# Performance work log

Hardware: AMD Instinct MI355X
Metric: run time of the kernel (lower is better)

## Reference

```python
import jax, jax.numpy as jnp
import numpy as np

B, L, E = 16, 1022, 1280
D, H, FF, NL = 512, 8, 2048, 4
DH = D // H
EPS = 1e-5


def layer_norm(x, s, b):
    m = jnp.mean(x, axis=-1, keepdims=True)
    v = jnp.mean(jnp.square(x - m), axis=-1, keepdims=True)
    return (x - m) * jax.lax.rsqrt(v + EPS) * s + b


def setup_inputs() -> dict:
    key = jax.random.key(0)
    ks = jax.random.split(key, 12)
    s = 0.02
    return {
        "embeddings": jax.random.normal(ks[0], (B, L, E), jnp.float32),
        "mask": jnp.ones((B, L), jnp.float32),
        "position": jnp.tile(jnp.arange(L, dtype=jnp.int32)[None, :], (B, 1)),
        "proj_w": jax.random.normal(ks[1], (D, E), jnp.float32) * s,
        "proj_b": jnp.zeros((D,), jnp.float32),
        "proj_ln_s": jnp.ones((D,), jnp.float32),
        "proj_ln_b": jnp.zeros((D,), jnp.float32),
        "ln1_s": jnp.ones((NL, D), jnp.float32),
        "ln1_b": jnp.zeros((NL, D), jnp.float32),
        "in_w": jax.random.normal(ks[2], (NL, 3 * D, D), jnp.float32) * s,
        "in_b": jnp.zeros((NL, 3 * D), jnp.float32),
        "out_w": jax.random.normal(ks[3], (NL, D, D), jnp.float32) * s,
        "out_b": jnp.zeros((NL, D), jnp.float32),
        "ln2_s": jnp.ones((NL, D), jnp.float32),
        "ln2_b": jnp.zeros((NL, D), jnp.float32),
        "w1": jax.random.normal(ks[4], (NL, FF, D), jnp.float32) * s,
        "b1": jnp.zeros((NL, FF), jnp.float32),
        "w2": jax.random.normal(ks[5], (NL, D, FF), jnp.float32) * s,
        "b2": jnp.zeros((NL, D), jnp.float32),
        "h1_w": jax.random.normal(ks[6], (128, 2 * D), jnp.float32) * s,
        "h1_b": jnp.zeros((128,), jnp.float32),
        "hln_s": jnp.ones((128,), jnp.float32),
        "hln_b": jnp.zeros((128,), jnp.float32),
        "h2_w": jax.random.normal(ks[7], (1, 128), jnp.float32) * s,
        "h2_b": jnp.zeros((1,), jnp.float32),
    }


def _rope_tables():
    inv_freq = 1.0 / (10000.0 ** (jnp.arange(0, DH, 2, dtype=jnp.float32) / DH))
    t = jnp.arange(L, dtype=jnp.float32)
    freqs = jnp.outer(t, inv_freq)          # [L, DH/2]
    emb = jnp.concatenate([freqs, freqs], axis=-1)  # [L, DH]
    return jnp.cos(emb), jnp.sin(emb)


def _rotate_half(x):
    x1, x2 = jnp.split(x, 2, axis=-1)
    return jnp.concatenate([-x2, x1], axis=-1)


def _apply_rope(x, cos, sin):
    # x: [B, L, D] -> per-head rotation -> [B, L, D]
    xh = x.reshape(B, L, H, DH)
    xh = xh * cos[None, :, None, :] + _rotate_half(xh) * sin[None, :, None, :]
    return xh.reshape(B, L, D)


def _forward(embeddings, mask, proj_w, proj_b, proj_ln_s, proj_ln_b,
             ln1_s, ln1_b, in_w, in_b, out_w, out_b, ln2_s, ln2_b,
             w1, b1, w2, b2, h1_w, h1_b, hln_s, hln_b, h2_w, h2_b):
    cos, sin = _rope_tables()
    x = layer_norm(embeddings @ proj_w.T + proj_b, proj_ln_s, proj_ln_b)  # [B,L,D]
    pad = mask <= 0  # True where padded (~mask.bool())
    scale = 1.0 / jnp.sqrt(jnp.float32(DH))
    for i in range(NL):
        n = layer_norm(x, ln1_s[i], ln1_b[i])
        q_in = _apply_rope(n, cos, sin)
        k_in = _apply_rope(n, cos, sin)
        v_in = n
        wq, wk, wv = jnp.split(in_w[i], 3, axis=0)
        bq, bk, bv = jnp.split(in_b[i], 3, axis=0)
        qh = (q_in @ wq.T + bq).reshape(B, L, H, DH)
        kh = (k_in @ wk.T + bk).reshape(B, L, H, DH)
        vh = (v_in @ wv.T + bv).reshape(B, L, H, DH)
        scores = jnp.einsum('blhd,bmhd->bhlm', qh, kh) * scale
        scores = jnp.where(pad[:, None, None, :], jnp.float32(-1e9), scores)
        attn = jax.nn.softmax(scores, axis=-1)
        o = jnp.einsum('bhlm,bmhd->blhd', attn, vh).reshape(B, L, D)
        x = x + (o @ out_w[i].T + out_b[i])
        n2 = layer_norm(x, ln2_s[i], ln2_b[i])
        x = x + (jax.nn.relu(n2 @ w1[i].T + b1[i]) @ w2[i].T + b2[i])
    # masked mean pool
    gctx = (x * mask[..., None]).sum(axis=1) / mask.sum(axis=1, keepdims=True)  # [B,D]
    combined = jnp.concatenate([x, jnp.broadcast_to(gctx[:, None, :], (B, L, D))], axis=-1)
    h = jax.nn.relu(layer_norm(combined @ h1_w.T + h1_b, hln_s, hln_b))
    logits = (h @ h2_w.T + h2_b).squeeze(-1)  # [B,L]
    return logits


def reference(embeddings, mask, position, proj_w, proj_b, proj_ln_s, proj_ln_b,
              ln1_s, ln1_b, in_w, in_b, out_w, out_b, ln2_s, ln2_b,
              w1, b1, w2, b2, h1_w, h1_b, hln_s, hln_b, h2_w, h2_b):
    # position is accepted for API parity but unused (as in the torch module)
    return _forward(embeddings, mask, proj_w, proj_b, proj_ln_s, proj_ln_b,
                    ln1_s, ln1_b, in_w, in_b, out_w, out_b, ln2_s, ln2_b,
                    w1, b1, w2, b2, h1_w, h1_b, hln_s, hln_b, h2_w, h2_b)
```

## Files before the change

kernel.cpp:

```cpp
#include <hip/hip_runtime.h>
#include <cstdint>
#include <cstddef>

#define B_   16
#define L_   1022
#define E_   1280
#define D_   512
#define H_   8
#define FF_  2048
#define NL_  4
#define DH_  64
#define BL_  (B_*L_)
#define EPS_ 1e-5f

typedef unsigned short u16;
typedef unsigned int   u32;
typedef float f32x4 __attribute__((ext_vector_type(4)));
typedef short s16x8 __attribute__((ext_vector_type(8)));

__device__ __forceinline__ u16 f2bf(float f) {
    u32 u = __builtin_bit_cast(u32, f);
    u += 0x7fffu + ((u >> 16) & 1u);
    return (u16)(u >> 16);
}
__device__ __forceinline__ float bf2f(u16 u) {
    return __builtin_bit_cast(float, (u32)u << 16);
}

__global__ __launch_bounds__(256)
void cast_k(const float* __restrict__ src, u16* __restrict__ dst, int n8) {
    int t = blockIdx.x * 256 + threadIdx.x;
    if (t >= n8) return;
    const float* s = src + (size_t)t * 8;
    float4 a = *(const float4*)(s);
    float4 b = *(const float4*)(s + 4);
    s16x8 o;
    o[0] = (short)f2bf(a.x); o[1] = (short)f2bf(a.y);
    o[2] = (short)f2bf(a.z); o[3] = (short)f2bf(a.w);
    o[4] = (short)f2bf(b.x); o[5] = (short)f2bf(b.y);
    o[6] = (short)f2bf(b.z); o[7] = (short)f2bf(b.w);
    *(s16x8*)(dst + (size_t)t * 8) = o;
}

__global__ __launch_bounds__(256)
void h1cast_k(const float* __restrict__ src, u16* __restrict__ dst) {
    int t = blockIdx.x * 256 + threadIdx.x;
    if (t >= 128 * 512 / 8) return;
    int row = t >> 6, c8 = (t & 63) << 3;
    const float* s = src + (size_t)row * 1024 + c8;
    float4 a = *(const float4*)(s);
    float4 b = *(const float4*)(s + 4);
    s16x8 o;
    o[0] = (short)f2bf(a.x); o[1] = (short)f2bf(a.y);
    o[2] = (short)f2bf(a.z); o[3] = (short)f2bf(a.w);
    o[4] = (short)f2bf(b.x); o[5] = (short)f2bf(b.y);
    o[6] = (short)f2bf(b.z); o[7] = (short)f2bf(b.w);
    *(s16x8*)(dst + (size_t)row * 512 + c8) = o;
}

__global__ void tables_k(float* __restrict__ ct, float* __restrict__ st) {
    int idx = blockIdx.x * blockDim.x + threadIdx.x;
    if (idx >= L_ * DH_) return;
    int l = idx / DH_;
    int d = idx % DH_;
    int j = d & 31;
    float invf = powf(10000.0f, -(float)(2 * j) / (float)DH_);
    float ang = (float)l * invf;
    ct[idx] = cosf(ang);
    st[idx] = sinf(ang);
}

template<bool RELU, bool RESID, bool OUTBF, bool ROWBIAS>
__global__ __launch_bounds__(256)
void mgemm_k(const u16* __restrict__ A, const u16* __restrict__ W,
             const float* __restrict__ bias, const float* __restrict__ resid,
             void* __restrict__ Cout, int M, int N, int K)
{
    constexpr int LDT = 72;
    __shared__ u16 As[128 * LDT];
    __shared__ u16 Ws[128 * LDT];
    const int nt = N >> 7;
    const int bx = blockIdx.x % nt;
    const int by = blockIdx.x / nt;
    const int m0 = by << 7, n0 = bx << 7;
    const int tid = threadIdx.x;
    const int lane = tid & 63, wid = tid >> 6;
    const int wr = wid >> 1, wc = wid & 1;
    const int lr = lane & 15, lk = lane >> 4;

    f32x4 acc[4][4];
#pragma unroll
    for (int m = 0; m < 4; m++)
#pragma unroll
        for (int n = 0; n < 4; n++) acc[m][n] = (f32x4)0.0f;

    for (int k0 = 0; k0 < K; k0 += 64) {
        s16x8 va[4], vw[4];
#pragma unroll
        for (int u = 0; u < 4; u++) {
            int ch = tid + (u << 8);
            int r = ch >> 3, c8 = (ch & 7) << 3;
            int ar = m0 + r; if (ar >= M) ar = M - 1;
            va[u] = *(const s16x8*)(A + (size_t)ar * K + k0 + c8);
            vw[u] = *(const s16x8*)(W + (size_t)(n0 + r) * K + k0 + c8);
        }
        __syncthreads();
#pragma unroll
        for (int u = 0; u < 4; u++) {
            int ch = tid + (u << 8);
            int r = ch >> 3, c8 = (ch & 7) << 3;
            *(s16x8*)&As[r * LDT + c8] = va[u];
            *(s16x8*)&Ws[r * LDT + c8] = vw[u];
        }
        __syncthreads();
#pragma unroll
        for (int kk = 0; kk < 2; kk++) {
            s16x8 af[4], bf[4];
#pragma unroll
            for (int m = 0; m < 4; m++)
                af[m] = *(const s16x8*)&As[(wr * 64 + m * 16 + lr) * LDT + kk * 32 + lk * 8];
#pragma unroll
            for (int n = 0; n < 4; n++)
                bf[n] = *(const s16x8*)&Ws[(wc * 64 + n * 16 + lr) * LDT + kk * 32 + lk * 8];
#pragma unroll
            for (int m = 0; m < 4; m++)
#pragma unroll
                for (int n = 0; n < 4; n++)
                    acc[m][n] = __builtin_amdgcn_mfma_f32_16x16x32_bf16(
                        af[m], bf[n], acc[m][n], 0, 0, 0);
        }
    }

    float bv[4];
    if constexpr (!ROWBIAS) {
#pragma unroll
        for (int n = 0; n < 4; n++) bv[n] = bias[n0 + wc * 64 + n * 16 + lr];
    }
#pragma unroll
    for (int m = 0; m < 4; m++) {
#pragma unroll
        for (int j = 0; j < 4; j++) {
            int row = m0 + wr * 64 + m * 16 + lk * 4 + j;
            if (row >= M) continue;
            const float* rb = nullptr;
            if constexpr (ROWBIAS) rb = bias + (size_t)(row / L_) * N;
#pragma unroll
            for (int n = 0; n < 4; n++) {
                int col = n0 + wc * 64 + n * 16 + lr;
                float c = acc[m][n][j];
                if constexpr (ROWBIAS) c += rb[col];
                else                   c += bv[n];
                if constexpr (RELU) c = fmaxf(c, 0.0f);
                if constexpr (RESID) c += resid[(size_t)row * N + col];
                if constexpr (OUTBF) ((u16*)Cout)[(size_t)row * N + col] = f2bf(c);
                else                 ((float*)Cout)[(size_t)row * N + col] = c;
            }
        }
    }
}

template<int DD, bool RELU, bool OUTBF>
__global__ __launch_bounds__(256)
void ln_k(const float* __restrict__ x, const float* __restrict__ s,
          const float* __restrict__ bb, void* __restrict__ out, int M)
{
    const int lane = threadIdx.x & 63;
    const int row = (blockIdx.x << 2) + (threadIdx.x >> 6);
    if (row >= M) return;
    const float* xr = x + (size_t)row * DD;
    constexpr int NV = DD / 64;
    float v[NV];
    if constexpr (NV == 8) {
        *(float4*)(v)     = *(const float4*)(xr + lane * 8);
        *(float4*)(v + 4) = *(const float4*)(xr + lane * 8 + 4);
    } else {
        float2 t = *(const float2*)(xr + lane * 2);
        v[0] = t.x; v[1] = t.y;
    }
    float sum = 0.f, sq = 0.f;
#pragma unroll
    for (int e = 0; e < NV; e++) { sum += v[e]; sq += v[e] * v[e]; }
#pragma unroll
    for (int msk = 1; msk < 64; msk <<= 1) {
        sum += __shfl_xor(sum, msk);
        sq  += __shfl_xor(sq, msk);
    }
    const float mean = sum * (1.0f / DD);
    const float var  = sq * (1.0f / DD) - mean * mean;
    const float rstd = rsqrtf(var + EPS_);
#pragma unroll
    for (int e = 0; e < NV; e++) {
        int d = lane * NV + e;
        float r = (v[e] - mean) * rstd * s[d] + bb[d];
        if constexpr (RELU) r = fmaxf(r, 0.0f);
        v[e] = r;
    }
    if constexpr (OUTBF) {
        u16* orow = (u16*)out + (size_t)row * DD;
        if constexpr (NV == 8) {
            s16x8 o;
#pragma unroll
            for (int e = 0; e < 8; e++) o[e] = (short)f2bf(v[e]);
            *(s16x8*)(orow + lane * 8) = o;
        } else {
            orow[lane * 2] = f2bf(v[0]); orow[lane * 2 + 1] = f2bf(v[1]);
        }
    } else {
        float* orow = (float*)out + (size_t)row * DD;
        if constexpr (NV == 8) {
            *(float4*)(orow + lane * 8)     = *(float4*)(v);
            *(float4*)(orow + lane * 8 + 4) = *(float4*)(v + 4);
        } else {
            float2 t; t.x = v[0]; t.y = v[1];
            *(float2*)(orow + lane * 2) = t;
        }
    }
}

__global__ __launch_bounds__(256)
void rope_k(const u16* __restrict__ n, const float* __restrict__ ct,
            const float* __restrict__ st, u16* __restrict__ r)
{
    int t = blockIdx.x * 256 + threadIdx.x;
    if (t >= BL_ * D_ / 8) return;
    int idx = t << 3;
    int l = (idx / D_) % L_;
    int d = idx & (D_ - 1);
    int dd = d & 63;
    s16x8 xv = *(const s16x8*)(n + idx);
    int pidx; float sgn;
    if (dd < 32) { pidx = idx + 32; sgn = -1.0f; }
    else         { pidx = idx - 32; sgn =  1.0f; }
    s16x8 pv = *(const s16x8*)(n + pidx);
    float4 c0 = *(const float4*)(ct + l * DH_ + dd);
    float4 c1 = *(const float4*)(ct + l * DH_ + dd + 4);
    float4 s0 = *(const float4*)(st + l * DH_ + dd);
    float4 s1 = *(const float4*)(st + l * DH_ + dd + 4);
    float cc[8] = {c0.x,c0.y,c0.z,c0.w,c1.x,c1.y,c1.z,c1.w};
    float ss[8] = {s0.x,s0.y,s0.z,s0.w,s1.x,s1.y,s1.z,s1.w};
    s16x8 o;
#pragma unroll
    for (int e = 0; e < 8; e++) {
        float xf = bf2f((u16)xv[e]);
        float pf = bf2f((u16)pv[e]);
        o[e] = (short)f2bf(xf * cc[e] + sgn * pf * ss[e]);
    }
    *(s16x8*)(r + idx) = o;
}

__global__ __launch_bounds__(256)
void attn_k(const u16* __restrict__ q, const u16* __restrict__ kk_,
            const u16* __restrict__ v, const float* __restrict__ mask,
            u16* __restrict__ o)
{
    constexpr int LDA = 68;
    __shared__ u16 Kt[64 * LDA];
    __shared__ u16 Vt[64 * LDA];
    __shared__ u16 Pl[64 * LDA];
    const int bh = blockIdx.x >> 4, qt = blockIdx.x & 15;
    const int b = bh >> 3, h = bh & 7;
    const int tid = threadIdx.x;
    const int lane = tid & 63, w = tid >> 6;
    const int lr = lane & 15, lg = lane >> 4;
    const size_t basebl = (size_t)b * L_;

    const int qrow = qt * 64 + w * 16 + lr;
    const int qclamp = qrow < L_ ? qrow : L_ - 1;
    s16x8 aq[2];
#pragma unroll
    for (int kk = 0; kk < 2; kk++)
        aq[kk] = *(const s16x8*)(q + (basebl + qclamp) * D_ + h * DH_ + kk * 32 + lg * 8);

    f32x4 oacc[4];
    float m_run[4], l_run[4];
#pragma unroll
    for (int n = 0; n < 4; n++) oacc[n] = (f32x4)0.0f;
#pragma unroll
    for (int j = 0; j < 4; j++) { m_run[j] = -1e30f; l_run[j] = 0.f; }

    for (int kt = 0; kt < 16; kt++) {
        __syncthreads();
#pragma unroll
        for (int u = 0; u < 2; u++) {
            int ch = tid + (u << 8);
            int key = ch >> 3, d8 = (ch & 7) << 3;
            int gk = kt * 64 + key;
            int gkc = gk < L_ ? gk : L_ - 1;
            s16x8 kv = *(const s16x8*)(kk_ + (basebl + gkc) * D_ + h * DH_ + d8);
            s16x8 vv = *(const s16x8*)(v   + (basebl + gkc) * D_ + h * DH_ + d8);
            *(s16x8*)&Kt[key * LDA + d8] = kv;
#pragma unroll
            for (int e = 0; e < 8; e++) Vt[(d8 + e) * LDA + key] = (u16)vv[e];
        }
        __syncthreads();

        f32x4 sacc[4];
#pragma unroll
        for (int n = 0; n < 4; n++) {
            sacc[n] = (f32x4)0.0f;
#pragma unroll
            for (int kk = 0; kk < 2; kk++) {
                s16x8 bk = *(const s16x8*)&Kt[(n * 16 + lr) * LDA + kk * 32 + lg * 8];
                sacc[n] = __builtin_amdgcn_mfma_f32_16x16x32_bf16(aq[kk], bk, sacc[n], 0, 0, 0);
            }
        }
        bool val[4];
#pragma unroll
        for (int n = 0; n < 4; n++) {
            int key = kt * 64 + n * 16 + lr;
            val[n] = (key < L_) && (mask[basebl + key] > 0.0f);
        }
#pragma unroll
        for (int j = 0; j < 4; j++) {
            float sv[4];
#pragma unroll
            for (int n = 0; n < 4; n++)
                sv[n] = val[n] ? sacc[n][j] * 0.125f : -1e30f;
            float tm = fmaxf(fmaxf(sv[0], sv[1]), fmaxf(sv[2], sv[3]));
#pragma unroll
            for (int msk = 1; msk <= 8; msk <<= 1) tm = fmaxf(tm, __shfl_xor(tm, msk));
            float nm = fmaxf(m_run[j], tm);
            float corr = __expf(m_run[j] - nm);
            m_run[j] = nm;
            float p[4], ts = 0.f;
#pragma unroll
            for (int n = 0; n < 4; n++) { p[n] = __expf(sv[n] - nm); ts += p[n]; }
#pragma unroll
            for (int msk = 1; msk <= 8; msk <<= 1) ts += __shfl_xor(ts, msk);
            l_run[j] = l_run[j] * corr + ts;
#pragma unroll
            for (int n = 0; n < 4; n++) {
                oacc[n][j] *= corr;
                Pl[(w * 16 + lg * 4 + j) * LDA + n * 16 + lr] = f2bf(p[n]);
            }
        }
#pragma unroll
        for (int kk = 0; kk < 2; kk++) {
            s16x8 ap = *(const s16x8*)&Pl[(w * 16 + lr) * LDA + kk * 32 + lg * 8];
#pragma unroll
            for (int n = 0; n < 4; n++) {
                s16x8 bv = *(const s16x8*)&Vt[(n * 16 + lr) * LDA + kk * 32 + lg * 8];
                oacc[n] = __builtin_amdgcn_mfma_f32_16x16x32_bf16(ap, bv, oacc[n], 0, 0, 0);
            }
        }
    }

#pragma unroll
    for (int j = 0; j < 4; j++) {
        int qr = qt * 64 + w * 16 + lg * 4 + j;
        if (qr >= L_) continue;
        float inv = 1.0f / l_run[j];
#pragma unroll
        for (int n = 0; n < 4; n++)
            o[(basebl + qr) * D_ + h * DH_ + n * 16 + lr] = f2bf(oacc[n][j] * inv);
    }
}

__global__ __launch_bounds__(512)
void pool_k(const float* __restrict__ x, const float* __restrict__ mask,
             float* __restrict__ g)
{
    const int b = blockIdx.x;
    const int d = threadIdx.x;
    float acc = 0.f, ms = 0.f;
    for (int l = 0; l < L_; l++) {
        float mv = mask[b * L_ + l];
        acc += x[((size_t)b * L_ + l) * D_ + d] * mv;
        ms += mv;
    }
    g[b * D_ + d] = acc / ms;
}

__global__ __launch_bounds__(256)
void gpart_k(const float* __restrict__ g, const float* __restrict__ h1w,
             const float* __restrict__ h1b, float* __restrict__ gp)
{
    const int lane = threadIdx.x & 63;
    const int gid = (blockIdx.x << 2) + (threadIdx.x >> 6);
    const int b = gid >> 7, j = gid & 127;
    const float* wr = h1w + (size_t)j * (2 * D_) + D_;
    const float* gr = g + b * D_;
    float4 a0 = *(const float4*)(gr + lane * 8);
    float4 a1 = *(const float4*)(gr + lane * 8 + 4);
    float4 w0 = *(const float4*)(wr + lane * 8);
    float4 w1v = *(const float4*)(wr + lane * 8 + 4);
    float acc = a0.x * w0.x + a0.y * w0.y + a0.z * w0.z + a0.w * w0.w
              + a1.x * w1v.x + a1.y * w1v.y + a1.z * w1v.z + a1.w * w1v.w;
#pragma unroll
    for (int msk = 1; msk < 64; msk <<= 1) acc += __shfl_xor(acc, msk);
    if (lane == 0) gp[b * 128 + j] = acc + h1b[j];
}

__global__ __launch_bounds__(256)
void logits_k(const float* __restrict__ h, const float* __restrict__ w,
              const float* __restrict__ bsc, float* __restrict__ out, int M)
{
    const int lane = threadIdx.x & 63;
    const int row = (blockIdx.x << 2) + (threadIdx.x >> 6);
    if (row >= M) return;
    float2 hv = *(const float2*)(h + (size_t)row * 128 + lane * 2);
    float2 wv = *(const float2*)(w + lane * 2);
    float acc = hv.x * wv.x + hv.y * wv.y;
#pragma unroll
    for (int msk = 1; msk < 64; msk <<= 1) acc += __shfl_xor(acc, msk);
    if (lane == 0) out[row] = acc + bsc[0];
}

extern "C" void kernel_launch(void* const* d_in, const int* in_sizes, int n_in,
                              void* d_out, int out_size, void* d_ws, size_t ws_size,
                              hipStream_t stream)
{
    const float* emb       = (const float*)d_in[0];
    const float* mask      = (const float*)d_in[1];
    const float* proj_w    = (const float*)d_in[3];
    const float* proj_b    = (const float*)d_in[4];
    const float* proj_ln_s = (const float*)d_in[5];
    const float* proj_ln_b = (const float*)d_in[6];
    const float* ln1_s     = (const float*)d_in[7];
    const float* ln1_b     = (const float*)d_in[8];
    const float* in_w      = (const float*)d_in[9];
    const float* in_b      = (const float*)d_in[10];
    const float* out_w     = (const float*)d_in[11];
    const float* out_b     = (const float*)d_in[12];
    const float* ln2_s     = (const float*)d_in[13];
    const float* ln2_b     = (const float*)d_in[14];
    const float* w1        = (const float*)d_in[15];
    const float* b1        = (const float*)d_in[16];
    const float* w2        = (const float*)d_in[17];
    const float* b2        = (const float*)d_in[18];
    const float* h1_w      = (const float*)d_in[19];
    const float* h1_b      = (const float*)d_in[20];
    const float* hln_s     = (const float*)d_in[21];
    const float* hln_b     = (const float*)d_in[22];
    const float* h2_w      = (const float*)d_in[23];
    const float* h2_b      = (const float*)d_in[24];
    float* out = (float*)d_out;

    float* ws = (float*)d_ws;
    const size_t S = (size_t)BL_ * D_;
    float* X  = ws;
    float* Rf = ws + S;
    u16* QB    = (u16*)(ws + S);
    u16* KB    = (u16*)(ws + S) + S;
    u16* VB    = (u16*)(ws + 2 * S);
    u16* NbB   = (u16*)(ws + 2 * S) + S;
    u16* FFb16 = (u16*)(ws + 3 * S);
    u16* RopeB = FFb16;
    u16* embB  = FFb16;
    u16* RB    = (u16*)(ws + 4 * S);
    u16* projwB = (u16*)(ws + 5 * S);
    u16* iwB  = projwB + 512 * 1280;
    u16* owB  = iwB + (size_t)NL_ * 3 * D_ * D_;
    u16* w1B  = owB + (size_t)NL_ * D_ * D_;
    u16* w2B  = w1B + (size_t)NL_ * FF_ * D_;
    u16* h1wB = w2B + (size_t)NL_ * D_ * FF_;
    float* CT = ws + 5 * S + 6651904;
    float* ST = CT + L_ * DH_;
    float* GC = ST + L_ * DH_;
    float* GP = GC + B_ * D_;
    float* Hb = Rf;

    const int MT = 128;
    const dim3 blk(256);
    const int lnGrid = (BL_ + 3) / 4;

    cast_k<<<(BL_ * E_ / 8 + 255) / 256, blk, 0, stream>>>(emb, embB, BL_ * E_ / 8);
    cast_k<<<(512 * 1280 / 8 + 255) / 256, blk, 0, stream>>>(proj_w, projwB, 512 * 1280 / 8);
    cast_k<<<(NL_ * 3 * D_ * D_ / 8 + 255) / 256, blk, 0, stream>>>(in_w, iwB, NL_ * 3 * D_ * D_ / 8);
    cast_k<<<(NL_ * D_ * D_ / 8 + 255) / 256, blk, 0, stream>>>(out_w, owB, NL_ * D_ * D_ / 8);
    cast_k<<<(NL_ * FF_ * D_ / 8 + 255) / 256, blk, 0, stream>>>(w1, w1B, NL_ * FF_ * D_ / 8);
    cast_k<<<(NL_ * D_ * FF_ / 8 + 255) / 256, blk, 0, stream>>>(w2, w2B, NL_ * D_ * FF_ / 8);
    h1cast_k<<<(128 * 512 / 8 + 255) / 256, blk, 0, stream>>>(h1_w, h1wB);
    tables_k<<<(L_ * DH_ + 255) / 256, blk, 0, stream>>>(CT, ST);

    mgemm_k<false,false,false,false><<<MT * (D_ / 128), blk, 0, stream>>>(
        embB, projwB, proj_b, nullptr, Rf, BL_, D_, E_);
    ln_k<D_,false,false><<<lnGrid, blk, 0, stream>>>(Rf, proj_ln_s, proj_ln_b, X, BL_);

    for (int i = 0; i < NL_; i++) {
        const u16* iw = iwB + (size_t)i * 3 * D_ * D_;
        const float* ib = in_b + (size_t)i * 3 * D_;
        ln_k<D_,false,true><<<lnGrid, blk, 0, stream>>>(X, ln1_s + i * D_, ln1_b + i * D_, NbB, BL_);
        mgemm_k<false,false,true,false><<<MT * 4, blk, 0, stream>>>(
            NbB, iw + 2 * D_ * D_, ib + 2 * D_, nullptr, VB, BL_, D_, D_);
        rope_k<<<(BL_ * D_ / 8 + 255) / 256, blk, 0, stream>>>(NbB, CT, ST, RopeB);
        mgemm_k<false,false,true,false><<<MT * 4, blk, 0, stream>>>(
            RopeB, iw, ib, nullptr, QB, BL_, D_, D_);
        mgemm_k<false,false,true,false><<<MT * 4, blk, 0, stream>>>(
            RopeB, iw + D_ * D_, ib + D_, nullptr, KB, BL_, D_, D_);
        attn_k<<<B_ * H_ * 16, blk, 0, stream>>>(QB, KB, VB, mask, RB);
        mgemm_k<false,true,false,false><<<MT * 4, blk, 0, stream>>>(
            RB, owB + (size_t)i * D_ * D_, out_b + i * D_, X, X, BL_, D_, D_);
        ln_k<D_,false,true><<<lnGrid, blk, 0, stream>>>(X, ln2_s + i * D_, ln2_b + i * D_, NbB, BL_);
        mgemm_k<true,false,true,false><<<MT * 16, blk, 0, stream>>>(
            NbB, w1B + (size_t)i * FF_ * D_, b1 + i * FF_, nullptr, FFb16, BL_, FF_, D_);
        mgemm_k<false,true,false,false><<<MT * 4, blk, 0, stream>>>(
            FFb16, w2B + (size_t)i * D_ * FF_, b2 + i * D_, X, X, BL_, D_, FF_);
    }

    pool_k<<<B_, dim3(512), 0, stream>>>(X, mask, GC);
    gpart_k<<<(B_ * 128) / 4, blk, 0, stream>>>(GC, h1_w, h1_b, GP);
    cast_k<<<(int)((S / 8 + 255) / 256), blk, 0, stream>>>(X, NbB, (int)(S / 8));
    mgemm_k<false,false,false,true><<<MT * 1, blk, 0, stream>>>(
        NbB, h1wB, GP, nullptr, Hb, BL_, 128, D_);
    ln_k<128,true,false><<<lnGrid, blk, 0, stream>>>(Hb, hln_s, hln_b, Hb, BL_);
    logits_k<<<lnGrid, blk, 0, stream>>>(Hb, h2_w, h2_b, out, BL_);
}
```

Before: 1.579 ms.

## Use direct global-to-LDS loads in GEMM, fuse Q/K projections, prefetch attention tiles

The GEMM now stages A and W tiles with global_load_lds straight into unpadded shared memory, skipping the register round trip. The separate Q and K projection GEMMs become one N=1024 GEMM writing an interleaved QK buffer, which saves a launch and re-reading the activations. The attention kernel prefetches the next K/V tile into registers while computing on the current one. The unpadded 64-wide LDS rows may cause bank conflicts on fragment reads, and the loads now sit right after the barrier instead of before it.

```diff
diff --git a/kernel.cpp b/kernel.cpp
--- a/kernel.cpp
+++ b/kernel.cpp
@@ -25,6 +25,13 @@
 }
 __device__ __forceinline__ float bf2f(u16 u) {
     return __builtin_bit_cast(float, (u32)u << 16);
+}
+
+__device__ __forceinline__ void gload_lds16(const u16* g, u16* l) {
+    __builtin_amdgcn_global_load_lds(
+        (const __attribute__((address_space(1))) void*)g,
+        (__attribute__((address_space(3))) void*)l,
+        16, 0, 0);
 }
 
 __global__ __launch_bounds__(256)
@@ -76,9 +83,8 @@
              const float* __restrict__ bias, const float* __restrict__ resid,
              void* __restrict__ Cout, int M, int N, int K)
 {
-    constexpr int LDT = 72;
-    __shared__ u16 As[128 * LDT];
-    __shared__ u16 Ws[128 * LDT];
+    __shared__ u16 As[128 * 64];
+    __shared__ u16 Ws[128 * 64];
     const int nt = N >> 7;
     const int bx = blockIdx.x % nt;
     const int by = blockIdx.x / nt;
@@ -95,22 +101,14 @@
         for (int n = 0; n < 4; n++) acc[m][n] = (f32x4)0.0f;
 
     for (int k0 = 0; k0 < K; k0 += 64) {
-        s16x8 va[4], vw[4];
+        __syncthreads();
 #pragma unroll
         for (int u = 0; u < 4; u++) {
             int ch = tid + (u << 8);
             int r = ch >> 3, c8 = (ch & 7) << 3;
             int ar = m0 + r; if (ar >= M) ar = M - 1;
-            va[u] = *(const s16x8*)(A + (size_t)ar * K + k0 + c8);
-            vw[u] = *(const s16x8*)(W + (size_t)(n0 + r) * K + k0 + c8);
-        }
-        __syncthreads();
-#pragma unroll
-        for (int u = 0; u < 4; u++) {
-            int ch = tid + (u << 8);
-            int r = ch >> 3, c8 = (ch & 7) << 3;
-            *(s16x8*)&As[r * LDT + c8] = va[u];
-            *(s16x8*)&Ws[r * LDT + c8] = vw[u];
+            gload_lds16(A + (size_t)ar * K + k0 + c8, &As[ch * 8]);
+            gload_lds16(W + (size_t)(n0 + r) * K + k0 + c8, &Ws[ch * 8]);
         }
         __syncthreads();
 #pragma unroll
@@ -118,10 +116,10 @@
             s16x8 af[4], bf[4];
 #pragma unroll
             for (int m = 0; m < 4; m++)
-                af[m] = *(const s16x8*)&As[(wr * 64 + m * 16 + lr) * LDT + kk * 32 + lk * 8];
+                af[m] = *(const s16x8*)&As[(wr * 64 + m * 16 + lr) * 64 + kk * 32 + lk * 8];
 #pragma unroll
             for (int n = 0; n < 4; n++)
-                bf[n] = *(const s16x8*)&Ws[(wc * 64 + n * 16 + lr) * LDT + kk * 32 + lk * 8];
+                bf[n] = *(const s16x8*)&Ws[(wc * 64 + n * 16 + lr) * 64 + kk * 32 + lk * 8];
 #pragma unroll
             for (int m = 0; m < 4; m++)
 #pragma unroll
@@ -249,9 +247,8 @@
 }
 
 __global__ __launch_bounds__(256)
-void attn_k(const u16* __restrict__ q, const u16* __restrict__ kk_,
-            const u16* __restrict__ v, const float* __restrict__ mask,
-            u16* __restrict__ o)
+void attn_k(const u16* __restrict__ qk, const u16* __restrict__ v,
+            const float* __restrict__ mask, u16* __restrict__ o)
 {
     constexpr int LDA = 68;
     __shared__ u16 Kt[64 * LDA];
@@ -269,7 +266,17 @@
     s16x8 aq[2];
 #pragma unroll
     for (int kk = 0; kk < 2; kk++)
-        aq[kk] = *(const s16x8*)(q + (basebl + qclamp) * D_ + h * DH_ + kk * 32 + lg * 8);
+        aq[kk] = *(const s16x8*)(qk + (basebl + qclamp) * 1024 + h * DH_ + kk * 32 + lg * 8);
+
+    s16x8 kreg[2], vreg[2];
+    const int pch_key[2] = { tid >> 3, (tid + 256) >> 3 };
+    const int pch_d8 = (tid & 7) << 3;
+#pragma unroll
+    for (int u = 0; u < 2; u++) {
+        int gk = pch_key[u]; if (gk >= L_) gk = L_ - 1;
+        kreg[u] = *(const s16x8*)(qk + (basebl + gk) * 1024 + 512 + h * DH_ + pch_d8);
+        vreg[u] = *(const s16x8*)(v  + (basebl + gk) * D_ + h * DH_ + pch_d8);
+    }
 
     f32x4 oacc[4];
     float m_run[4], l_run[4];
@@ -282,17 +289,19 @@
         __syncthreads();
 #pragma unroll
         for (int u = 0; u < 2; u++) {
-            int ch = tid + (u << 8);
-            int key = ch >> 3, d8 = (ch & 7) << 3;
-            int gk = kt * 64 + key;
-            int gkc = gk < L_ ? gk : L_ - 1;
-            s16x8 kv = *(const s16x8*)(kk_ + (basebl + gkc) * D_ + h * DH_ + d8);
-            s16x8 vv = *(const s16x8*)(v   + (basebl + gkc) * D_ + h * DH_ + d8);
-            *(s16x8*)&Kt[key * LDA + d8] = kv;
-#pragma unroll
-            for (int e = 0; e < 8; e++) Vt[(d8 + e) * LDA + key] = (u16)vv[e];
+            *(s16x8*)&Kt[pch_key[u] * LDA + pch_d8] = kreg[u];
+#pragma unroll
+            for (int e = 0; e < 8; e++) Vt[(pch_d8 + e) * LDA + pch_key[u]] = (u16)vreg[u][e];
         }
         __syncthreads();
+        if (kt < 15) {
+#pragma unroll
+            for (int u = 0; u < 2; u++) {
+                int gk = (kt + 1) * 64 + pch_key[u]; if (gk >= L_) gk = L_ - 1;
+                kreg[u] = *(const s16x8*)(qk + (basebl + gk) * 1024 + 512 + h * DH_ + pch_d8);
+                vreg[u] = *(const s16x8*)(v  + (basebl + gk) * D_ + h * DH_ + pch_d8);
+            }
+        }
 
         f32x4 sacc[4];
 #pragma unroll
@@ -440,8 +449,7 @@
     const size_t S = (size_t)BL_ * D_;
     float* X  = ws;
     float* Rf = ws + S;
-    u16* QB    = (u16*)(ws + S);
-    u16* KB    = (u16*)(ws + S) + S;
+    u16* QKB   = (u16*)(ws + S);
     u16* VB    = (u16*)(ws + 2 * S);
     u16* NbB   = (u16*)(ws + 2 * S) + S;
     u16* FFb16 = (u16*)(ws + 3 * S);
@@ -484,11 +492,9 @@
         mgemm_k<false,false,true,false><<<MT * 4, blk, 0, stream>>>(
             NbB, iw + 2 * D_ * D_, ib + 2 * D_, nullptr, VB, BL_, D_, D_);
         rope_k<<<(BL_ * D_ / 8 + 255) / 256, blk, 0, stream>>>(NbB, CT, ST, RopeB);
-        mgemm_k<false,false,true,false><<<MT * 4, blk, 0, stream>>>(
-            RopeB, iw, ib, nullptr, QB, BL_, D_, D_);
-        mgemm_k<false,false,true,false><<<MT * 4, blk, 0, stream>>>(
-            RopeB, iw + D_ * D_, ib + D_, nullptr, KB, BL_, D_, D_);
-        attn_k<<<B_ * H_ * 16, blk, 0, stream>>>(QB, KB, VB, mask, RB);
+        mgemm_k<false,false,true,false><<<MT * 8, blk, 0, stream>>>(
+            RopeB, iw, ib, nullptr, QKB, BL_, 1024, D_);
+        attn_k<<<B_ * H_ * 16, blk, 0, stream>>>(QKB, VB, mask, RB);
         mgemm_k<false,true,false,false><<<MT * 4, blk, 0, stream>>>(
             RB, owB + (size_t)i * D_ * D_, out_b + i * D_, X, X, BL_, D_, D_);
         ln_k<D_,false,true><<<lnGrid, blk, 0, stream>>>(X, ln2_s + i * D_, ln2_b + i * D_, NbB, BL_);
```

New measurement: 1.705 ms. +8.0%, slower.

## Fuse Q/K projections into one GEMM and process two query tiles per attention block

Applied to the files above, without the earlier changes.

The separate Q and K projection GEMMs become a single N=1024 GEMM writing an interleaved QK buffer. The attention kernel now handles 128 query rows per block (two 16-row groups per wave), so each staged K/V tile is reused twice and the kernel launches half as many blocks. The softmax row sum is no longer computed with shuffle reductions; an extra MFMA against a vector of ones accumulates it instead. The trade-offs are more registers per thread, fewer blocks to fill the GPU, and a denominator taken from bf16-rounded probabilities.

```diff
diff --git a/kernel.cpp b/kernel.cpp
--- a/kernel.cpp
+++ b/kernel.cpp
@@ -249,110 +249,124 @@
 }
 
 __global__ __launch_bounds__(256)
-void attn_k(const u16* __restrict__ q, const u16* __restrict__ kk_,
-            const u16* __restrict__ v, const float* __restrict__ mask,
-            u16* __restrict__ o)
+void attn_k(const u16* __restrict__ qk, const u16* __restrict__ v,
+            const float* __restrict__ mask, u16* __restrict__ o)
 {
     constexpr int LDA = 68;
     __shared__ u16 Kt[64 * LDA];
     __shared__ u16 Vt[64 * LDA];
     __shared__ u16 Pl[64 * LDA];
-    const int bh = blockIdx.x >> 4, qt = blockIdx.x & 15;
+    const int bh = blockIdx.x >> 3, qt = blockIdx.x & 7;
     const int b = bh >> 3, h = bh & 7;
     const int tid = threadIdx.x;
     const int lane = tid & 63, w = tid >> 6;
     const int lr = lane & 15, lg = lane >> 4;
     const size_t basebl = (size_t)b * L_;
 
-    const int qrow = qt * 64 + w * 16 + lr;
-    const int qclamp = qrow < L_ ? qrow : L_ - 1;
-    s16x8 aq[2];
-#pragma unroll
-    for (int kk = 0; kk < 2; kk++)
-        aq[kk] = *(const s16x8*)(q + (basebl + qclamp) * D_ + h * DH_ + kk * 32 + lg * 8);
-
-    f32x4 oacc[4];
-    float m_run[4], l_run[4];
-#pragma unroll
-    for (int n = 0; n < 4; n++) oacc[n] = (f32x4)0.0f;
-#pragma unroll
-    for (int j = 0; j < 4; j++) { m_run[j] = -1e30f; l_run[j] = 0.f; }
+    s16x8 aq[2][2];
+#pragma unroll
+    for (int g = 0; g < 2; g++) {
+        int qrow = qt * 128 + w * 32 + g * 16 + lr;
+        int qc = qrow < L_ ? qrow : L_ - 1;
+#pragma unroll
+        for (int kk = 0; kk < 2; kk++)
+            aq[g][kk] = *(const s16x8*)(qk + (basebl + qc) * 1024 + h * DH_ + kk * 32 + lg * 8);
+    }
+
+    s16x8 bones;
+#pragma unroll
+    for (int e = 0; e < 8; e++) bones[e] = (short)0x3F80;
+
+    f32x4 oacc[2][4], ocs[2];
+    float m_run[2][4];
+#pragma unroll
+    for (int g = 0; g < 2; g++) {
+        ocs[g] = (f32x4)0.0f;
+#pragma unroll
+        for (int n = 0; n < 4; n++) oacc[g][n] = (f32x4)0.0f;
+#pragma unroll
+        for (int j = 0; j < 4; j++) m_run[g][j] = -1e30f;
+    }
+
+    const int st_key = tid >> 3;
+    const int st_d8 = (tid & 7) << 3;
 
     for (int kt = 0; kt < 16; kt++) {
         __syncthreads();
 #pragma unroll
         for (int u = 0; u < 2; u++) {
-            int ch = tid + (u << 8);
-            int key = ch >> 3, d8 = (ch & 7) << 3;
-            int gk = kt * 64 + key;
-            int gkc = gk < L_ ? gk : L_ - 1;
-            s16x8 kv = *(const s16x8*)(kk_ + (basebl + gkc) * D_ + h * DH_ + d8);
-            s16x8 vv = *(const s16x8*)(v   + (basebl + gkc) * D_ + h * DH_ + d8);
-            *(s16x8*)&Kt[key * LDA + d8] = kv;
-#pragma unroll
-            for (int e = 0; e < 8; e++) Vt[(d8 + e) * LDA + key] = (u16)vv[e];
+            int key = st_key + u * 32;
+            int gk = kt * 64 + key; if (gk >= L_) gk = L_ - 1;
+            s16x8 kv = *(const s16x8*)(qk + (basebl + gk) * 1024 + 512 + h * DH_ + st_d8);
+            s16x8 vv = *(const s16x8*)(v  + (basebl + gk) * D_ + h * DH_ + st_d8);
+            *(s16x8*)&Kt[key * LDA + st_d8] = kv;
+#pragma unroll
+            for (int e = 0; e < 8; e++) Vt[(st_d8 + e) * LDA + key] = (u16)vv[e];
         }
         __syncthreads();
 
-        f32x4 sacc[4];
-#pragma unroll
-        for (int n = 0; n < 4; n++) {
-            sacc[n] = (f32x4)0.0f;
-#pragma unroll
-            for (int kk = 0; kk < 2; kk++) {
-                s16x8 bk = *(const s16x8*)&Kt[(n * 16 + lr) * LDA + kk * 32 + lg * 8];
-                sacc[n] = __builtin_amdgcn_mfma_f32_16x16x32_bf16(aq[kk], bk, sacc[n], 0, 0, 0);
-            }
-        }
         bool val[4];
 #pragma unroll
         for (int n = 0; n < 4; n++) {
             int key = kt * 64 + n * 16 + lr;
             val[n] = (key < L_) && (mask[basebl + key] > 0.0f);
         }
+
+#pragma unroll
+        for (int g = 0; g < 2; g++) {
+            f32x4 sacc[4];
+#pragma unroll
+            for (int n = 0; n < 4; n++) {
+                sacc[n] = (f32x4)0.0f;
+#pragma unroll
+                for (int kk = 0; kk < 2; kk++) {
+                    s16x8 bk = *(const s16x8*)&Kt[(n * 16 + lr) * LDA + kk * 32 + lg * 8];
+                    sacc[n] = __builtin_amdgcn_mfma_f32_16x16x32_bf16(aq[g][kk], bk, sacc[n], 0, 0, 0);
+                }
+            }
+#pragma unroll
+            for (int j = 0; j < 4; j++) {
+                float sv[4];
+#pragma unroll
+                for (int n = 0; n < 4; n++)
+                    sv[n] = val[n] ? sacc[n][j] * 0.125f : -1e30f;
+                float tm = fmaxf(fmaxf(sv[0], sv[1]), fmaxf(sv[2], sv[3]));
+#pragma unroll
+                for (int msk = 1; msk <= 8; msk <<= 1) tm = fmaxf(tm, __shfl_xor(tm, msk));
+                float nm = fmaxf(m_run[g][j], tm);
+                float corr = __expf(m_run[g][j] - nm);
+                m_run[g][j] = nm;
+                ocs[g][j] *= corr;
+#pragma unroll
+                for (int n = 0; n < 4; n++) {
+                    oacc[g][n][j] *= corr;
+                    Pl[(w * 16 + lg * 4 + j) * LDA + n * 16 + lr] = f2bf(__expf(sv[n] - nm));
+                }
+            }
+#pragma unroll
+            for (int kk = 0; kk < 2; kk++) {
+                s16x8 ap = *(const s16x8*)&Pl[(w * 16 + lr) * LDA + kk * 32 + lg * 8];
+#pragma unroll
+                for (int n = 0; n < 4; n++) {
+                    s16x8 bv = *(const s16x8*)&Vt[(n * 16 + lr) * LDA + kk * 32 + lg * 8];
+                    oacc[g][n] = __builtin_amdgcn_mfma_f32_16x16x32_bf16(ap, bv, oacc[g][n], 0, 0, 0);
+                }
+                ocs[g] = __builtin_amdgcn_mfma_f32_16x16x32_bf16(ap, bones, ocs[g], 0, 0, 0);
+            }
+        }
+    }
+
+#pragma unroll
+    for (int g = 0; g < 2; g++) {
 #pragma unroll
         for (int j = 0; j < 4; j++) {
-            float sv[4];
+            int qr = qt * 128 + w * 32 + g * 16 + lg * 4 + j;
+            if (qr >= L_) continue;
+            float inv = 1.0f / ocs[g][j];
 #pragma unroll
             for (int n = 0; n < 4; n++)
-                sv[n] = val[n] ? sacc[n][j] * 0.125f : -1e30f;
-            float tm = fmaxf(fmaxf(sv[0], sv[1]), fmaxf(sv[2], sv[3]));
-#pragma unroll
-            for (int msk = 1; msk <= 8; msk <<= 1) tm = fmaxf(tm, __shfl_xor(tm, msk));
-            float nm = fmaxf(m_run[j], tm);
-            float corr = __expf(m_run[j] - nm);
-            m_run[j] = nm;
-            float p[4], ts = 0.f;
-#pragma unroll
-            for (int n = 0; n < 4; n++) { p[n] = __expf(sv[n] - nm); ts += p[n]; }
-#pragma unroll
-            for (int msk = 1; msk <= 8; msk <<= 1) ts += __shfl_xor(ts, msk);
-            l_run[j] = l_run[j] * corr + ts;
-#pragma unroll
-            for (int n = 0; n < 4; n++) {
-                oacc[n][j] *= corr;
-                Pl[(w * 16 + lg * 4 + j) * LDA + n * 16 + lr] = f2bf(p[n]);
-            }
-        }
-#pragma unroll
-        for (int kk = 0; kk < 2; kk++) {
-            s16x8 ap = *(const s16x8*)&Pl[(w * 16 + lr) * LDA + kk * 32 + lg * 8];
-#pragma unroll
-            for (int n = 0; n < 4; n++) {
-                s16x8 bv = *(const s16x8*)&Vt[(n * 16 + lr) * LDA + kk * 32 + lg * 8];
-                oacc[n] = __builtin_amdgcn_mfma_f32_16x16x32_bf16(ap, bv, oacc[n], 0, 0, 0);
-            }
-        }
-    }
-
-#pragma unroll
-    for (int j = 0; j < 4; j++) {
-        int qr = qt * 64 + w * 16 + lg * 4 + j;
-        if (qr >= L_) continue;
-        float inv = 1.0f / l_run[j];
-#pragma unroll
-        for (int n = 0; n < 4; n++)
-            o[(basebl + qr) * D_ + h * DH_ + n * 16 + lr] = f2bf(oacc[n][j] * inv);
+                o[(basebl + qr) * D_ + h * DH_ + n * 16 + lr] = f2bf(oacc[g][n][j] * inv);
+        }
     }
 }
 
@@ -440,8 +454,7 @@
     const size_t S = (size_t)BL_ * D_;
     float* X  = ws;
     float* Rf = ws + S;
-    u16* QB    = (u16*)(ws + S);
-    u16* KB    = (u16*)(ws + S) + S;
+    u16* QKB   = (u16*)(ws + S);
     u16* VB    = (u16*)(ws + 2 * S);
     u16* NbB   = (u16*)(ws + 2 * S) + S;
     u16* FFb16 = (u16*)(ws + 3 * S);
@@ -484,11 +497,9 @@
         mgemm_k<false,false,true,false><<<MT * 4, blk, 0, stream>>>(
             NbB, iw + 2 * D_ * D_, ib + 2 * D_, nullptr, VB, BL_, D_, D_);
         rope_k<<<(BL_ * D_ / 8 + 255) / 256, blk, 0, stream>>>(NbB, CT, ST, RopeB);
-        mgemm_k<false,false,true,false><<<MT * 4, blk, 0, stream>>>(
-            RopeB, iw, ib, nullptr, QB, BL_, D_, D_);
-        mgemm_k<false,false,true,false><<<MT * 4, blk, 0, stream>>>(
-            RopeB, iw + D_ * D_, ib + D_, nullptr, KB, BL_, D_, D_);
-        attn_k<<<B_ * H_ * 16, blk, 0, stream>>>(QB, KB, VB, mask, RB);
+        mgemm_k<false,false,true,false><<<MT * 8, blk, 0, stream>>>(
+            RopeB, iw, ib, nullptr, QKB, BL_, 1024, D_);
+        attn_k<<<B_ * H_ * 8, blk, 0, stream>>>(QKB, VB, mask, RB);
         mgemm_k<false,true,false,false><<<MT * 4, blk, 0, stream>>>(
             RB, owB + (size_t)i * D_ * D_, out_b + i * D_, X, X, BL_, D_, D_);
         ln_k<D_,false,true><<<lnGrid, blk, 0, stream>>>(X, ln2_s + i * D_, ln2_b + i * D_, NbB, BL_);
```

Result: no change. 1.576 ms (-0.2%).
